# Performance work log

Measured on AMD Instinct MI355X. Metric: run time of the kernel, lower is better.

The kernel has to match this reference:

```python
import jax, jax.numpy as jnp
import numpy as np

N_NODES = 40000
N_EDGES = 640000
HIDDEN = 128


def setup_inputs() -> dict:
    key = jax.random.key(0)
    k_h, k_w, k_b, k_src, k_dst = jax.random.split(key, 5)
    h = jax.random.normal(k_h, (N_NODES, HIDDEN), dtype=jnp.float32)
    # nn.Linear(hidden_dim, hidden_dim): weight [out, in], bias [out]
    W = jax.random.normal(k_w, (HIDDEN, HIDDEN), dtype=jnp.float32) * (1.0 / np.sqrt(HIDDEN))
    b = jax.random.normal(k_b, (HIDDEN,), dtype=jnp.float32) * 0.01
    src = jax.random.randint(k_src, (N_EDGES,), 0, N_NODES, dtype=jnp.int32)
    dst = jax.random.randint(k_dst, (N_EDGES,), 0, N_NODES, dtype=jnp.int32)
    return {"h": h, "W": W, "b": b, "src": src, "dst": dst}


def reference(h, W, b, src, dst):
    n = h.shape[0]
    # message: gather source node features; reduce: mailbox sum == segment-sum by dst
    agg = jax.ops.segment_sum(h[src], dst, num_segments=n)  # [N, D]
    updated = agg @ W.T + b  # merge_linner
    # DGL update_all only writes nodes with >=1 incoming edge; others keep old h
    indeg = jax.ops.segment_sum(jnp.ones(src.shape, dtype=h.dtype), dst, num_segments=n)
    return jnp.where((indeg > 0)[:, None], updated, h)
```

## Files before the change

### kernel.cpp

```cpp
#include <hip/hip_runtime.h>
#include <hip/hip_bf16.h>

static constexpr int HIDDEN = 128;

using bf16x8 = __attribute__((ext_vector_type(8))) __bf16;
using f32x4 = __attribute__((ext_vector_type(4))) float;

__device__ inline ushort f2bf(float x) {
  __hip_bfloat16 t = __float2bfloat16(x);
  return *reinterpret_cast<ushort*>(&t);
}


__global__ void __launch_bounds__(256) hist_kernel(
    const int* __restrict__ dst, int* __restrict__ counts, int n_edges) {
  int i = blockIdx.x * 256 + threadIdx.x;
  if (i < n_edges) atomicAdd(&counts[dst[i]], 1);
}

__global__ void __launch_bounds__(256) scanA_kernel(
    const int* __restrict__ counts, int* __restrict__ tilesums, int n) {
  const int t = threadIdx.x;
  const int base = blockIdx.x * 1024 + t * 4;
  int s = 0;
  if (base + 3 < n) {
    int4 v = *reinterpret_cast<const int4*>(counts + base);
    s = v.x + v.y + v.z + v.w;
  } else {
    for (int j = 0; j < 4; ++j)
      if (base + j < n) s += counts[base + j];
  }
  for (int off = 1; off < 64; off <<= 1) s += __shfl_xor(s, off, 64);
  __shared__ int wp[4];
  if ((t & 63) == 0) wp[t >> 6] = s;
  __syncthreads();
  if (t == 0) tilesums[blockIdx.x] = wp[0] + wp[1] + wp[2] + wp[3];
}

__global__ void __launch_bounds__(64) scanB_kernel(int* tilesums, int nt) {
  int t = threadIdx.x;
  int v = (t < nt) ? tilesums[t] : 0;
  int orig = v;
  for (int off = 1; off < 64; off <<= 1) {
    int u = __shfl_up(v, off, 64);
    if (t >= off) v += u;
  }
  if (t < nt) tilesums[t] = v - orig;
}

__global__ void __launch_bounds__(256) scanC_kernel(
    const int* __restrict__ counts, const int* __restrict__ tileprefix,
    int* __restrict__ offsets, int n) {
  const int t = threadIdx.x;
  const int base = blockIdx.x * 1024 + t * 4;
  int4 v = {0, 0, 0, 0};
  const bool full = (base + 3 < n);
  if (full) {
    v = *reinterpret_cast<const int4*>(counts + base);
  } else {
    if (base + 0 < n) v.x = counts[base + 0];
    if (base + 1 < n) v.y = counts[base + 1];
    if (base + 2 < n) v.z = counts[base + 2];
    if (base + 3 < n) v.w = counts[base + 3];
  }
  const int s = v.x + v.y + v.z + v.w;
  int inc = s;
  for (int off = 1; off < 64; off <<= 1) {
    int u = __shfl_up(inc, off, 64);
    if ((t & 63) >= off) inc += u;
  }
  const int excl = inc - s;
  __shared__ int wp[4];
  if ((t & 63) == 63) wp[t >> 6] = inc;
  __syncthreads();
  int wbase = 0;
  for (int w = 0; w < (t >> 6); ++w) wbase += wp[w];
  int p = tileprefix[blockIdx.x] + wbase + excl;
  if (full) {
    int4 o;
    o.x = p;
    o.y = p + v.x;
    o.z = p + v.x + v.y;
    o.w = p + v.x + v.y + v.z;
    *reinterpret_cast<int4*>(offsets + base) = o;
  } else {
    int run = p;
    if (base + 0 < n) { offsets[base + 0] = run; run += v.x; }
    if (base + 1 < n) { offsets[base + 1] = run; run += v.y; }
    if (base + 2 < n) { offsets[base + 2] = run; run += v.z; }
    if (base + 3 < n) { offsets[base + 3] = run; }
  }
}

__global__ void __launch_bounds__(256) fill_kernel(
    const int* __restrict__ src, const int* __restrict__ dst,
    int* __restrict__ offsets, int* __restrict__ esorted, int n_edges) {
  int i = blockIdx.x * 256 + threadIdx.x;
  if (i < n_edges) {
    int pos = atomicAdd(&offsets[dst[i]], 1);
    esorted[pos] = src[i];
  }
}

__global__ void __launch_bounds__(256) wconv_kernel(
    const float* __restrict__ W, ushort* __restrict__ wbf) {
  int i = blockIdx.x * 256 + threadIdx.x;
  if (i < HIDDEN * HIDDEN) wbf[i] = f2bf(W[i]);
}

__global__ void __launch_bounds__(256) transform_mfma_kernel(
    const float* __restrict__ h, const ushort* __restrict__ wbf,
    ushort* __restrict__ hW, int n_nodes) {
  const int wave = threadIdx.x >> 6;
  const int lane = threadIdx.x & 63;
  const int r16 = lane & 15;
  const int kq = lane >> 4;
  const int kbase = kq * 8;
  const int base = blockIdx.x * 64 + wave * 16;

  int arow = base + r16;
  if (arow >= n_nodes) arow = n_nodes - 1;
  const float* hrow = h + (size_t)arow * HIDDEN;

  bf16x8 a[4];
#pragma unroll
  for (int ks = 0; ks < 4; ++ks) {
    const float4 u = *reinterpret_cast<const float4*>(hrow + ks * 32 + kbase);
    const float4 v =
        *reinterpret_cast<const float4*>(hrow + ks * 32 + kbase + 4);
    bf16x8 t;
    t[0] = (__bf16)u.x;
    t[1] = (__bf16)u.y;
    t[2] = (__bf16)u.z;
    t[3] = (__bf16)u.w;
    t[4] = (__bf16)v.x;
    t[5] = (__bf16)v.y;
    t[6] = (__bf16)v.z;
    t[7] = (__bf16)v.w;
    a[ks] = t;
  }

  const int drow0 = base + kq * 4;
#pragma unroll
  for (int ct = 0; ct < 8; ++ct) {
    const ushort* wrow = wbf + (size_t)(ct * 16 + r16) * HIDDEN;
    f32x4 acc = {0.f, 0.f, 0.f, 0.f};
#pragma unroll
    for (int ks = 0; ks < 4; ++ks) {
      bf16x8 bfrag =
          *reinterpret_cast<const bf16x8*>(wrow + ks * 32 + kbase);
      acc = __builtin_amdgcn_mfma_f32_16x16x32_bf16(a[ks], bfrag, acc, 0, 0, 0);
    }
#pragma unroll
    for (int r = 0; r < 4; ++r) {
      int nrow = drow0 + r;
      if (nrow < n_nodes)
        hW[(size_t)nrow * HIDDEN + ct * 16 + r16] = f2bf(acc[r]);
    }
  }
}

__global__ void __launch_bounds__(256) gather_sum_kernel(
    const ushort* __restrict__ hW, const float* __restrict__ h,
    const float* __restrict__ b, const int* __restrict__ counts,
    const int* __restrict__ ends, const int* __restrict__ esorted,
    float* __restrict__ out, int n_nodes) {
  const int lane = threadIdx.x & 15;
  const int group = threadIdx.x >> 4;
  const int f0 = lane * 8;
  const int node = blockIdx.x * 16 + group;
  if (node >= n_nodes) return;

  const int deg = counts[node];
  float4 o0, o1;
  if (deg == 0) {
    o0 = *reinterpret_cast<const float4*>(h + (size_t)node * HIDDEN + f0);
    o1 = *reinterpret_cast<const float4*>(h + (size_t)node * HIDDEN + f0 + 4);
  } else {
    const int start = ends[node] - deg;
    float4 A = {0.f, 0.f, 0.f, 0.f};
    float4 B = {0.f, 0.f, 0.f, 0.f};
    for (int base = 0; base < deg; base += 16) {
      int sreg = 0;
      if (base + lane < deg) sreg = esorted[start + base + lane];
      const int m = min(16, deg - base);
#pragma unroll 8
      for (int jj = 0; jj < m; ++jj) {
        int s = __shfl(sreg, jj, 16);
        uint4 v =
            *reinterpret_cast<const uint4*>(hW + (size_t)s * HIDDEN + f0);
        A.x += __uint_as_float(v.x << 16);
        A.y += __uint_as_float(v.x & 0xffff0000u);
        A.z += __uint_as_float(v.y << 16);
        A.w += __uint_as_float(v.y & 0xffff0000u);
        B.x += __uint_as_float(v.z << 16);
        B.y += __uint_as_float(v.z & 0xffff0000u);
        B.z += __uint_as_float(v.w << 16);
        B.w += __uint_as_float(v.w & 0xffff0000u);
      }
    }
    const float4 b0 = *reinterpret_cast<const float4*>(b + f0);
    const float4 b1 = *reinterpret_cast<const float4*>(b + f0 + 4);
    o0 = {A.x + b0.x, A.y + b0.y, A.z + b0.z, A.w + b0.w};
    o1 = {B.x + b1.x, B.y + b1.y, B.z + b1.z, B.w + b1.w};
  }
  *reinterpret_cast<float4*>(out + (size_t)node * HIDDEN + f0) = o0;
  *reinterpret_cast<float4*>(out + (size_t)node * HIDDEN + f0 + 4) = o1;
}


__global__ void __launch_bounds__(1024) scan_kernel(
    const int* __restrict__ counts, int* __restrict__ offsets, int n) {
  __shared__ int part[1024];
  const int t = threadIdx.x;
  const int C = (n + 1023) / 1024;
  const int base = t * C;
  int sum = 0;
  for (int j = 0; j < C; ++j) {
    int idx = base + j;
    if (idx < n) sum += counts[idx];
  }
  part[t] = sum;
  __syncthreads();
  for (int s = 1; s < 1024; s <<= 1) {
    int v = (t >= s) ? part[t - s] : 0;
    __syncthreads();
    part[t] += v;
    __syncthreads();
  }
  int run = part[t] - sum;
  for (int j = 0; j < C; ++j) {
    int idx = base + j;
    if (idx < n) {
      offsets[idx] = run;
      run += counts[idx];
    }
  }
}

__global__ void __launch_bounds__(256, 2) gather_update_kernel(
    const float* __restrict__ h, const float* __restrict__ W,
    const float* __restrict__ b, const int* __restrict__ counts,
    const int* __restrict__ ends, const int* __restrict__ esorted,
    float* __restrict__ out, int n_nodes) {
  __shared__ float Wt[HIDDEN][HIDDEN];
  for (int i = threadIdx.x; i < HIDDEN * HIDDEN / 4; i += 256) {
    int idx = i * 4;
    int j = idx >> 7;
    int k = idx & 127;
    float4 w = *reinterpret_cast<const float4*>(W + j * HIDDEN + k);
    Wt[k + 0][j] = w.x;
    Wt[k + 1][j] = w.y;
    Wt[k + 2][j] = w.z;
    Wt[k + 3][j] = w.w;
  }
  __syncthreads();
  const int lane = threadIdx.x & 31;
  const int group = threadIdx.x >> 5;
  const int j0 = lane * 4;
  const float4 bias = *reinterpret_cast<const float4*>(b + j0);
  const int nb = (n_nodes + 7) >> 3;
  for (int batch = blockIdx.x; batch < nb; batch += gridDim.x) {
    int node = batch * 8 + group;
    if (node >= n_nodes) continue;
    const int deg = counts[node];
    float4 res;
    if (deg == 0) {
      res = reinterpret_cast<const float4*>(h + (size_t)node * HIDDEN)[lane];
    } else {
      const int start = ends[node] - deg;
      float4 acc = {0.f, 0.f, 0.f, 0.f};
      for (int basei = 0; basei < deg; basei += 32) {
        int sreg = 0;
        if (basei + lane < deg) sreg = esorted[start + basei + lane];
        const int m = min(32, deg - basei);
        for (int jj = 0; jj < m; ++jj) {
          int s = __shfl(sreg, jj, 32);
          float4 v =
              reinterpret_cast<const float4*>(h + (size_t)s * HIDDEN)[lane];
          acc.x += v.x;
          acc.y += v.y;
          acc.z += v.z;
          acc.w += v.w;
        }
      }
      const float* av = reinterpret_cast<const float*>(&acc);
      float4 o = bias;
#pragma unroll
      for (int k = 0; k < HIDDEN; ++k) {
        float aval = __shfl(av[k & 3], k >> 2, 32);
        float4 w = *reinterpret_cast<const float4*>(&Wt[k][j0]);
        o.x = fmaf(aval, w.x, o.x);
        o.y = fmaf(aval, w.y, o.y);
        o.z = fmaf(aval, w.z, o.z);
        o.w = fmaf(aval, w.w, o.w);
      }
      res = o;
    }
    reinterpret_cast<float4*>(out + (size_t)node * HIDDEN)[lane] = res;
  }
}


extern "C" void kernel_launch(void* const* d_in, const int* in_sizes, int n_in,
                              void* d_out, int out_size, void* d_ws, size_t ws_size,
                              hipStream_t stream) {
  const float* h = (const float*)d_in[0];
  const float* W = (const float*)d_in[1];
  const float* b = (const float*)d_in[2];
  const int* src = (const int*)d_in[3];
  const int* dst = (const int*)d_in[4];
  float* out = (float*)d_out;
  const int n_nodes = in_sizes[0] / HIDDEN;
  const int n_edges = in_sizes[3];

  const int n_round = (n_nodes + 1023) & ~1023;
  const int nt = n_round / 1024;
  const int eblocks = (n_edges + 255) / 256;

  int* counts = (int*)d_ws;
  int* offsets = counts + n_round;
  int* tilesums = offsets + n_round;
  int* esorted = tilesums + 64;
  size_t off_bytes = ((size_t)(2 * n_round + 64 + n_edges) * 4 + 15) & ~15ull;
  ushort* hW = (ushort*)((char*)d_ws + off_bytes);
  size_t wbf_off =
      (off_bytes + (size_t)n_nodes * HIDDEN * 2 + 15) & ~15ull;
  ushort* wbf = (ushort*)((char*)d_ws + wbf_off);
  const size_t need_full = wbf_off + (size_t)HIDDEN * HIDDEN * 2;

  if (ws_size >= need_full && nt <= 64) {
    hipMemsetAsync(counts, 0, (size_t)n_nodes * sizeof(int), stream);
    hist_kernel<<<eblocks, 256, 0, stream>>>(dst, counts, n_edges);
    scanA_kernel<<<nt, 256, 0, stream>>>(counts, tilesums, n_nodes);
    scanB_kernel<<<1, 64, 0, stream>>>(tilesums, nt);
    scanC_kernel<<<nt, 256, 0, stream>>>(counts, tilesums, offsets, n_nodes);
    fill_kernel<<<eblocks, 256, 0, stream>>>(src, dst, offsets, esorted,
                                             n_edges);
    wconv_kernel<<<(HIDDEN * HIDDEN + 255) / 256, 256, 0, stream>>>(W, wbf);
    const int tblocks = (n_nodes + 63) / 64;
    transform_mfma_kernel<<<tblocks, 256, 0, stream>>>(h, wbf, hW, n_nodes);
    const int gblocks = (n_nodes + 15) / 16;
    gather_sum_kernel<<<gblocks, 256, 0, stream>>>(hW, h, b, counts, offsets,
                                                   esorted, out, n_nodes);
  } else {
    hipMemsetAsync(counts, 0, (size_t)n_nodes * sizeof(int), stream);
    hist_kernel<<<eblocks, 256, 0, stream>>>(dst, counts, n_edges);
    scan_kernel<<<1, 1024, 0, stream>>>(counts, offsets, n_nodes);
    fill_kernel<<<eblocks, 256, 0, stream>>>(src, dst, offsets, esorted,
                                             n_edges);
    gather_update_kernel<<<512, 256, 0, stream>>>(h, W, b, counts, offsets,
                                                  esorted, out, n_nodes);
  }
}
```

Before: 186.3 us.

## Fuse small kernels, vectorize edge passes, stage MFMA output via LDS

```diff
diff --git a/kernel.cpp b/kernel.cpp
--- a/kernel.cpp
+++ b/kernel.cpp
@@ -5,17 +5,39 @@
 
 using bf16x8 = __attribute__((ext_vector_type(8))) __bf16;
 using f32x4 = __attribute__((ext_vector_type(4))) float;
+using ushort8v = __attribute__((ext_vector_type(8))) ushort;
 
 __device__ inline ushort f2bf(float x) {
   __hip_bfloat16 t = __float2bfloat16(x);
   return *reinterpret_cast<ushort*>(&t);
 }
 
-
-__global__ void __launch_bounds__(256) hist_kernel(
-    const int* __restrict__ dst, int* __restrict__ counts, int n_edges) {
-  int i = blockIdx.x * 256 + threadIdx.x;
-  if (i < n_edges) atomicAdd(&counts[dst[i]], 1);
+__global__ void __launch_bounds__(256) hist_wconv_kernel(
+    const int* __restrict__ dst, int* __restrict__ counts, int n_edges,
+    int nbh, const float* __restrict__ W, ushort* __restrict__ wbf) {
+  if (blockIdx.x < nbh) {
+    int i = (blockIdx.x * 256 + threadIdx.x) * 4;
+    if (i + 3 < n_edges) {
+      int4 d = *reinterpret_cast<const int4*>(dst + i);
+      atomicAdd(&counts[d.x], 1);
+      atomicAdd(&counts[d.y], 1);
+      atomicAdd(&counts[d.z], 1);
+      atomicAdd(&counts[d.w], 1);
+    } else {
+      for (int j = i; j < n_edges; ++j) atomicAdd(&counts[dst[j]], 1);
+    }
+  } else {
+    int i = ((blockIdx.x - nbh) * 256 + threadIdx.x) * 4;
+    if (i < HIDDEN * HIDDEN) {
+      float4 w = *reinterpret_cast<const float4*>(W + i);
+      ushort4 u;
+      u.x = f2bf(w.x);
+      u.y = f2bf(w.y);
+      u.z = f2bf(w.z);
+      u.w = f2bf(w.w);
+      *reinterpret_cast<ushort4*>(wbf + i) = u;
+    }
+  }
 }
 
 __global__ void __launch_bounds__(256) scanA_kernel(
@@ -37,21 +59,22 @@
   if (t == 0) tilesums[blockIdx.x] = wp[0] + wp[1] + wp[2] + wp[3];
 }
 
-__global__ void __launch_bounds__(64) scanB_kernel(int* tilesums, int nt) {
-  int t = threadIdx.x;
-  int v = (t < nt) ? tilesums[t] : 0;
-  int orig = v;
-  for (int off = 1; off < 64; off <<= 1) {
-    int u = __shfl_up(v, off, 64);
-    if (t >= off) v += u;
-  }
-  if (t < nt) tilesums[t] = v - orig;
-}
-
 __global__ void __launch_bounds__(256) scanC_kernel(
-    const int* __restrict__ counts, const int* __restrict__ tileprefix,
-    int* __restrict__ offsets, int n) {
+    const int* __restrict__ counts, const int* __restrict__ tilesums,
+    int* __restrict__ offsets, int n, int nt) {
+  __shared__ int tp[64];
   const int t = threadIdx.x;
+  if (t < 64) {
+    int v = (t < nt) ? tilesums[t] : 0;
+    int orig = v;
+    for (int off = 1; off < 64; off <<= 1) {
+      int u = __shfl_up(v, off, 64);
+      if (t >= off) v += u;
+    }
+    tp[t] = v - orig;
+  }
+  __syncthreads();
+
   const int base = blockIdx.x * 1024 + t * 4;
   int4 v = {0, 0, 0, 0};
   const bool full = (base + 3 < n);
@@ -75,7 +98,7 @@
   __syncthreads();
   int wbase = 0;
   for (int w = 0; w < (t >> 6); ++w) wbase += wp[w];
-  int p = tileprefix[blockIdx.x] + wbase + excl;
+  int p = tp[blockIdx.x] + wbase + excl;
   if (full) {
     int4 o;
     o.x = p;
@@ -95,22 +118,31 @@
 __global__ void __launch_bounds__(256) fill_kernel(
     const int* __restrict__ src, const int* __restrict__ dst,
     int* __restrict__ offsets, int* __restrict__ esorted, int n_edges) {
-  int i = blockIdx.x * 256 + threadIdx.x;
-  if (i < n_edges) {
-    int pos = atomicAdd(&offsets[dst[i]], 1);
-    esorted[pos] = src[i];
-  }
-}
-
-__global__ void __launch_bounds__(256) wconv_kernel(
-    const float* __restrict__ W, ushort* __restrict__ wbf) {
-  int i = blockIdx.x * 256 + threadIdx.x;
-  if (i < HIDDEN * HIDDEN) wbf[i] = f2bf(W[i]);
+  int i = (blockIdx.x * 256 + threadIdx.x) * 4;
+  if (i + 3 < n_edges) {
+    int4 s = *reinterpret_cast<const int4*>(src + i);
+    int4 d = *reinterpret_cast<const int4*>(dst + i);
+    int p0 = atomicAdd(&offsets[d.x], 1);
+    int p1 = atomicAdd(&offsets[d.y], 1);
+    int p2 = atomicAdd(&offsets[d.z], 1);
+    int p3 = atomicAdd(&offsets[d.w], 1);
+    esorted[p0] = s.x;
+    esorted[p1] = s.y;
+    esorted[p2] = s.z;
+    esorted[p3] = s.w;
+  } else {
+    for (int j = i; j < n_edges; ++j) {
+      int pos = atomicAdd(&offsets[dst[j]], 1);
+      esorted[pos] = src[j];
+    }
+  }
 }
 
 __global__ void __launch_bounds__(256) transform_mfma_kernel(
     const float* __restrict__ h, const ushort* __restrict__ wbf,
     ushort* __restrict__ hW, int n_nodes) {
+  constexpr int COLP = 136;
+  __shared__ ushort tile[4][16][COLP];
   const int wave = threadIdx.x >> 6;
   const int lane = threadIdx.x & 63;
   const int r16 = lane & 15;
@@ -140,22 +172,27 @@
     a[ks] = t;
   }
 
-  const int drow0 = base + kq * 4;
 #pragma unroll
   for (int ct = 0; ct < 8; ++ct) {
     const ushort* wrow = wbf + (size_t)(ct * 16 + r16) * HIDDEN;
     f32x4 acc = {0.f, 0.f, 0.f, 0.f};
 #pragma unroll
     for (int ks = 0; ks < 4; ++ks) {
-      bf16x8 bfrag =
-          *reinterpret_cast<const bf16x8*>(wrow + ks * 32 + kbase);
+      bf16x8 bfrag = *reinterpret_cast<const bf16x8*>(wrow + ks * 32 + kbase);
       acc = __builtin_amdgcn_mfma_f32_16x16x32_bf16(a[ks], bfrag, acc, 0, 0, 0);
     }
 #pragma unroll
-    for (int r = 0; r < 4; ++r) {
-      int nrow = drow0 + r;
-      if (nrow < n_nodes)
-        hW[(size_t)nrow * HIDDEN + ct * 16 + r16] = f2bf(acc[r]);
+    for (int r = 0; r < 4; ++r)
+      tile[wave][kq * 4 + r][ct * 16 + r16] = f2bf(acc[r]);
+  }
+#pragma unroll
+  for (int it = 0; it < 4; ++it) {
+    const int row = it * 4 + (lane >> 4);
+    const int cb = r16 * 8;
+    const int nrow = base + row;
+    if (nrow < n_nodes) {
+      ushort8v v = *reinterpret_cast<const ushort8v*>(&tile[wave][row][cb]);
+      *reinterpret_cast<ushort8v*>(hW + (size_t)nrow * HIDDEN + cb) = v;
     }
   }
 }
@@ -172,23 +209,26 @@
   if (node >= n_nodes) return;
 
   const int deg = counts[node];
-  float4 o0, o1;
+  f32x4 o0, o1;
   if (deg == 0) {
-    o0 = *reinterpret_cast<const float4*>(h + (size_t)node * HIDDEN + f0);
-    o1 = *reinterpret_cast<const float4*>(h + (size_t)node * HIDDEN + f0 + 4);
+    float4 t0 = *reinterpret_cast<const float4*>(h + (size_t)node * HIDDEN + f0);
+    float4 t1 =
+        *reinterpret_cast<const float4*>(h + (size_t)node * HIDDEN + f0 + 4);
+    o0 = {t0.x, t0.y, t0.z, t0.w};
+    o1 = {t1.x, t1.y, t1.z, t1.w};
   } else {
     const int start = ends[node] - deg;
     float4 A = {0.f, 0.f, 0.f, 0.f};
     float4 B = {0.f, 0.f, 0.f, 0.f};
     for (int base = 0; base < deg; base += 16) {
       int sreg = 0;
-      if (base + lane < deg) sreg = esorted[start + base + lane];
+      if (base + lane < deg)
+        sreg = __builtin_nontemporal_load(esorted + start + base + lane);
       const int m = min(16, deg - base);
 #pragma unroll 8
       for (int jj = 0; jj < m; ++jj) {
         int s = __shfl(sreg, jj, 16);
-        uint4 v =
-            *reinterpret_cast<const uint4*>(hW + (size_t)s * HIDDEN + f0);
+        uint4 v = *reinterpret_cast<const uint4*>(hW + (size_t)s * HIDDEN + f0);
         A.x += __uint_as_float(v.x << 16);
         A.y += __uint_as_float(v.x & 0xffff0000u);
         A.z += __uint_as_float(v.y << 16);
@@ -204,10 +244,28 @@
     o0 = {A.x + b0.x, A.y + b0.y, A.z + b0.z, A.w + b0.w};
     o1 = {B.x + b1.x, B.y + b1.y, B.z + b1.z, B.w + b1.w};
   }
-  *reinterpret_cast<float4*>(out + (size_t)node * HIDDEN + f0) = o0;
-  *reinterpret_cast<float4*>(out + (size_t)node * HIDDEN + f0 + 4) = o1;
-}
-
+  __builtin_nontemporal_store(
+      o0, reinterpret_cast<f32x4*>(out + (size_t)node * HIDDEN + f0));
+  __builtin_nontemporal_store(
+      o1, reinterpret_cast<f32x4*>(out + (size_t)node * HIDDEN + f0 + 4));
+}
+
+
+__global__ void __launch_bounds__(256) hist_kernel(
+    const int* __restrict__ dst, int* __restrict__ counts, int n_edges) {
+  int i = blockIdx.x * 256 + threadIdx.x;
+  if (i < n_edges) atomicAdd(&counts[dst[i]], 1);
+}
+
+__global__ void __launch_bounds__(256) fill1_kernel(
+    const int* __restrict__ src, const int* __restrict__ dst,
+    int* __restrict__ offsets, int* __restrict__ esorted, int n_edges) {
+  int i = blockIdx.x * 256 + threadIdx.x;
+  if (i < n_edges) {
+    int pos = atomicAdd(&offsets[dst[i]], 1);
+    esorted[pos] = src[i];
+  }
+}
 
 __global__ void __launch_bounds__(1024) scan_kernel(
     const int* __restrict__ counts, int* __restrict__ offsets, int n) {
@@ -316,7 +374,7 @@
 
   const int n_round = (n_nodes + 1023) & ~1023;
   const int nt = n_round / 1024;
-  const int eblocks = (n_edges + 255) / 256;
+  const int eblocks4 = (n_edges + 1023) / 1024;
 
   int* counts = (int*)d_ws;
   int* offsets = counts + n_round;
@@ -324,31 +382,32 @@
   int* esorted = tilesums + 64;
   size_t off_bytes = ((size_t)(2 * n_round + 64 + n_edges) * 4 + 15) & ~15ull;
   ushort* hW = (ushort*)((char*)d_ws + off_bytes);
-  size_t wbf_off =
-      (off_bytes + (size_t)n_nodes * HIDDEN * 2 + 15) & ~15ull;
+  size_t wbf_off = (off_bytes + (size_t)n_nodes * HIDDEN * 2 + 15) & ~15ull;
   ushort* wbf = (ushort*)((char*)d_ws + wbf_off);
   const size_t need_full = wbf_off + (size_t)HIDDEN * HIDDEN * 2;
 
   if (ws_size >= need_full && nt <= 64) {
-    hipMemsetAsync(counts, 0, (size_t)n_nodes * sizeof(int), stream);
-    hist_kernel<<<eblocks, 256, 0, stream>>>(dst, counts, n_edges);
+    (void)hipMemsetAsync(counts, 0, (size_t)n_nodes * sizeof(int), stream);
+    const int wblocks = (HIDDEN * HIDDEN + 1023) / 1024;
+    hist_wconv_kernel<<<eblocks4 + wblocks, 256, 0, stream>>>(
+        dst, counts, n_edges, eblocks4, W, wbf);
     scanA_kernel<<<nt, 256, 0, stream>>>(counts, tilesums, n_nodes);
-    scanB_kernel<<<1, 64, 0, stream>>>(tilesums, nt);
-    scanC_kernel<<<nt, 256, 0, stream>>>(counts, tilesums, offsets, n_nodes);
-    fill_kernel<<<eblocks, 256, 0, stream>>>(src, dst, offsets, esorted,
-                                             n_edges);
-    wconv_kernel<<<(HIDDEN * HIDDEN + 255) / 256, 256, 0, stream>>>(W, wbf);
+    scanC_kernel<<<nt, 256, 0, stream>>>(counts, tilesums, offsets, n_nodes,
+                                         nt);
+    fill_kernel<<<eblocks4, 256, 0, stream>>>(src, dst, offsets, esorted,
+                                              n_edges);
     const int tblocks = (n_nodes + 63) / 64;
     transform_mfma_kernel<<<tblocks, 256, 0, stream>>>(h, wbf, hW, n_nodes);
     const int gblocks = (n_nodes + 15) / 16;
     gather_sum_kernel<<<gblocks, 256, 0, stream>>>(hW, h, b, counts, offsets,
                                                    esorted, out, n_nodes);
   } else {
-    hipMemsetAsync(counts, 0, (size_t)n_nodes * sizeof(int), stream);
+    (void)hipMemsetAsync(counts, 0, (size_t)n_nodes * sizeof(int), stream);
+    const int eblocks = (n_edges + 255) / 256;
     hist_kernel<<<eblocks, 256, 0, stream>>>(dst, counts, n_edges);
     scan_kernel<<<1, 1024, 0, stream>>>(counts, offsets, n_nodes);
-    fill_kernel<<<eblocks, 256, 0, stream>>>(src, dst, offsets, esorted,
-                                             n_edges);
+    fill1_kernel<<<eblocks, 256, 0, stream>>>(src, dst, offsets, esorted,
+                                              n_edges);
     gather_update_kernel<<<512, 256, 0, stream>>>(h, W, b, counts, offsets,
                                                   esorted, out, n_nodes);
   }
```

Result: no change. 184.0 us (-1.2%).
